# Kernel tuning notes

Measured on AMD Instinct MI355X. Metric: run time of the kernel, lower is better.

## Reference

```python
import jax, jax.numpy as jnp
import numpy as np

D = 768       # input_dim / model width
H = 3072      # expert hidden width (init arg 'output_dim')
E = 8         # num_experts
K = 2         # top_k
NOISE_STD = 0.1
B, S = 2, 1024


def setup_inputs() -> dict:
    key = jax.random.key(0)
    ks = jax.random.split(key, 16)
    sd = lambda fan_in: 1.0 / np.sqrt(fan_in)
    return {
        "x": jax.random.normal(ks[0], (B, S, D), dtype=jnp.float32),
        "noise": jax.random.normal(ks[1], (B, S, E), dtype=jnp.float32),
        # router
        "Wr": jax.random.normal(ks[2], (D, E), dtype=jnp.float32) * sd(D),
        "br": jnp.zeros((E,), dtype=jnp.float32),
        # stacked expert FFNs: d -> h -> d
        "W1": jax.random.normal(ks[3], (E, D, H), dtype=jnp.float32) * sd(D),
        "b1": jnp.zeros((E, H), dtype=jnp.float32),
        "W2": jax.random.normal(ks[4], (E, H, D), dtype=jnp.float32) * sd(H),
        "b2": jnp.zeros((E, D), dtype=jnp.float32),
        # shared expert
        "Ws1": jax.random.normal(ks[5], (D, H), dtype=jnp.float32) * sd(D),
        "bs1": jnp.zeros((H,), dtype=jnp.float32),
        "Ws2": jax.random.normal(ks[6], (H, D), dtype=jnp.float32) * sd(H),
        "bs2": jnp.zeros((D,), dtype=jnp.float32),
        # mixing scalars (alpha trainable, beta frozen in torch)
        "alpha": jnp.float32(0.3),
        "beta": jnp.float32(0.7),
    }


def reference(x, noise, Wr, br, W1, b1, W2, b2, Ws1, bs1, Ws2, bs2, alpha, beta):
    b, s, d = x.shape
    xt = x.reshape(-1, d)                       # [T, D]
    nt = noise.reshape(-1, E)                   # [T, E]
    T = xt.shape[0]

    # router: noisy logits -> top-k -> softmax over selected experts only
    logits = xt @ Wr + br + NOISE_STD * nt      # [T, E]
    top_vals, top_idx = jax.lax.top_k(logits, K)  # [T, K]
    top_w = jax.nn.softmax(top_vals, axis=-1)     # softmax over -inf-masked logits == softmax over top-k
    gates = jnp.zeros((T, E), dtype=x.dtype).at[jnp.arange(T)[:, None], top_idx].set(top_w)  # [T, E], 0 elsewhere

    # experts (dense over E; non-selected contributions are zeroed by gates)
    h = jax.nn.leaky_relu(jnp.einsum('td,edh->teh', xt, W1) + b1, negative_slope=0.01)  # [T, E, H]
    y = jnp.einsum('teh,ehd->ted', h, W2) + b2                                          # [T, E, D]
    moe_out = jnp.einsum('ted,te->td', y, gates)                                        # [T, D]

    # shared expert
    sh = jax.nn.leaky_relu(xt @ Ws1 + bs1, negative_slope=0.01)
    shared_out = sh @ Ws2 + bs2                                                         # [T, D]

    w = jax.nn.softmax(jnp.stack([alpha, beta]))
    out = shared_out * w[0] + moe_out * w[1]
    return out.reshape(b, s, d)
```

## Files before the change

kernel.cpp:

```cpp
#include <hip/hip_runtime.h>
#include <hip/hip_bf16.h>
#include <cstdio>
#include <cstdint>

#define TNUM 2048
#define DDIM 768
#define HDIM 3072
#define ENUM 8

#define WAITVM(N) asm volatile("s_waitcnt vmcnt(" #N ")" ::: "memory")
#define WAITLGKM() asm volatile("s_waitcnt lgkmcnt(0)" ::: "memory")
#define MEMFENCE() asm volatile("" ::: "memory")

typedef __attribute__((ext_vector_type(8))) __bf16 bf16x8;
typedef __attribute__((ext_vector_type(4))) float f32x4;

__device__ __forceinline__ unsigned short f2bf(float f) {
    __bf16 h = (__bf16)f;
    unsigned short u;
    __builtin_memcpy(&u, &h, 2);
    return u;
}

__device__ __forceinline__ void async_cp16(const unsigned short* g, unsigned short* l) {
    __builtin_amdgcn_global_load_lds((const __attribute__((address_space(1))) void*)g,
                                     (__attribute__((address_space(3))) void*)l,
                                     16, 0, 0);
}

__device__ __forceinline__ void transpose_tile(const float* __restrict__ in,
                                               unsigned short* __restrict__ out,
                                               int R, int C, int c0, int r0,
                                               unsigned int* tileT32) {
    int tid = threadIdx.x;
    int l15 = tid & 15;
    int g = tid >> 4;
    int par = (g >> 1) & 1;
    int hf = g & 1;
    int cb = hf * 64 + l15 * 4;
    const float* src = in + (size_t)(r0 + (g >> 1)) * C + c0 + cb;
    float4 v[16];
    #pragma unroll
    for (int p = 0; p < 16; p++)
        v[p] = *(const float4*)(src + (size_t)p * 8 * C);
    #pragma unroll
    for (int p = 0; p < 16; p++) {
        int unit = p * 16 + g;
        unsigned int m01 = (unsigned int)f2bf(v[p].x) | ((unsigned int)f2bf(v[p].y) << 16);
        unsigned int m23 = (unsigned int)f2bf(v[p].z) | ((unsigned int)f2bf(v[p].w) << 16);
        unsigned int o01 = __shfl_xor(m01, 32);
        unsigned int o23 = __shfl_xor(m23, 32);
        unsigned int wA = par ? ((o23 & 0xffffu) | (m23 << 16))
                              : ((m01 & 0xffffu) | (o01 << 16));
        unsigned int wB = par ? ((o23 >> 16) | (m23 & 0xffff0000u))
                              : ((m01 >> 16) | (o01 & 0xffff0000u));
        int ca = cb + par * 2;
        int rp = unit >> 2;
        int cq = ca >> 2;
        int woff = 4 * (((rp >> 2) + 3 * cq) & 15) + (((rp & 3) + cq) & 3);
        tileT32[ca * 68 + woff] = wA;
        tileT32[(ca + 1) * 68 + woff] = wB;
    }
    __syncthreads();
    uint4 Wv[8];
    #pragma unroll
    for (int p = 0; p < 8; p++) {
        int cc = p * 16 + g;
        int cqp = cc >> 2;
        Wv[p] = *(const uint4*)&tileT32[cc * 68 + 4 * ((l15 + 3 * cqp) & 15)];
    }
    #pragma unroll
    for (int p = 0; p < 8; p++) {
        int cc = p * 16 + g;
        int cqp = cc >> 2;
        unsigned int a0 = Wv[p].x, a1 = Wv[p].y, a2 = Wv[p].z, a3 = Wv[p].w;
        int rsel = cqp & 3;
        if (rsel & 1) { unsigned int t = a0; a0 = a1; a1 = a2; a2 = a3; a3 = t; }
        if (rsel & 2) { unsigned int t0 = a0, t1 = a1; a0 = a2; a1 = a3; a2 = t0; a3 = t1; }
        uint4 ov; ov.x = a0; ov.y = a1; ov.z = a2; ov.w = a3;
        *(uint4*)(out + (size_t)(c0 + cc) * R + r0 + l15 * 8) = ov;
    }
}

__global__ __launch_bounds__(256, 4)
void pre_kernel(const float* __restrict__ x, const float* __restrict__ noise,
                const float* __restrict__ Wr, const float* __restrict__ br,
                const float* __restrict__ W2, const float* __restrict__ Ws2,
                unsigned short* __restrict__ W2t, unsigned short* __restrict__ Ws2t,
                unsigned short* __restrict__ xb,
                int* __restrict__ counts, int* __restrict__ list,
                int* __restrict__ inv, float* __restrict__ tokp) {
    __shared__ __align__(16) unsigned int tileT32[128 * 68];
    int b = blockIdx.x;
    if (b < 1296) {
        int m = b / 144, t = b % 144;
        const float* in     = (m < 8) ? (W2 + (size_t)m * HDIM * DDIM) : Ws2;
        unsigned short* out = (m < 8) ? (W2t + (size_t)m * DDIM * HDIM) : Ws2t;
        transpose_tile(in, out, HDIM, DDIM, (t % 6) * 128, (t / 6) * 128, tileT32);
        return;
    }
    if (b < 2064) {
        int i = ((b - 1296) * 256 + threadIdx.x) * 8;
        float4 a = *(const float4*)(x + i);
        float4 bb = *(const float4*)(x + i + 4);
        ushort4 lo = make_ushort4(f2bf(a.x), f2bf(a.y), f2bf(a.z), f2bf(a.w));
        ushort4 hi = make_ushort4(f2bf(bb.x), f2bf(bb.y), f2bf(bb.z), f2bf(bb.w));
        *(ushort4*)(xb + i) = lo;
        *(ushort4*)(xb + i + 4) = hi;
        return;
    }
    int lane = threadIdx.x & 63;
    int t = (b - 2064) * 4 + (threadIdx.x >> 6);
    float acc[8];
    #pragma unroll
    for (int e = 0; e < 8; e++) acc[e] = 0.f;
    #pragma unroll
    for (int i = 0; i < 12; i++) {
        int d = i * 64 + lane;
        float xv = x[t * DDIM + d];
        float4 w0 = *(const float4*)(Wr + d * 8);
        float4 w1 = *(const float4*)(Wr + d * 8 + 4);
        acc[0] += xv * w0.x; acc[1] += xv * w0.y; acc[2] += xv * w0.z; acc[3] += xv * w0.w;
        acc[4] += xv * w1.x; acc[5] += xv * w1.y; acc[6] += xv * w1.z; acc[7] += xv * w1.w;
    }
    #pragma unroll
    for (int e = 0; e < 8; e++) {
        #pragma unroll
        for (int off2 = 32; off2 >= 1; off2 >>= 1)
            acc[e] += __shfl_xor(acc[e], off2, 64);
    }
    if (lane == 0) {
        float lg[8];
        #pragma unroll
        for (int e = 0; e < 8; e++) lg[e] = acc[e] + br[e] + 0.1f * noise[t * 8 + e];
        int e0 = 0;
        #pragma unroll
        for (int e = 1; e < 8; e++) if (lg[e] > lg[e0]) e0 = e;
        int e1 = -1;
        #pragma unroll
        for (int e = 0; e < 8; e++) if (e != e0 && (e1 < 0 || lg[e] > lg[e1])) e1 = e;
        float m = fmaxf(lg[e0], lg[e1]);
        float p0 = expf(lg[e0] - m), p1 = expf(lg[e1] - m);
        float inv_s = 1.f / (p0 + p1);
        int s0 = atomicAdd(&counts[e0], 1);
        list[e0 * TNUM + s0] = t;
        int s1 = atomicAdd(&counts[e1], 1);
        list[e1 * TNUM + s1] = t;
        inv[t * 2 + 0] = (e0 << 16) | s0;
        inv[t * 2 + 1] = (e1 << 16) | s1;
        tokp[t * 2 + 0] = p0 * inv_s;
        tokp[t * 2 + 1] = p1 * inv_s;
    }
}

__global__ __launch_bounds__(256, 3)
void ffn1_kernel(const unsigned short* __restrict__ xb,
                 const float* __restrict__ W1,
                 const float* __restrict__ Ws1,
                 const float* __restrict__ b1, const float* __restrict__ bs1,
                 const int* __restrict__ counts, const int* __restrict__ list,
                 unsigned short* __restrict__ hbuf) {
    __shared__ __align__(16) unsigned short As[2][512 * 8];
    __shared__ __align__(16) unsigned int Bs32[2048];

    int j = blockIdx.z * 8 + blockIdx.x;
    int y = blockIdx.y;
    int mt0 = y / 6, ntl = y % 6;

    int offv[8];
    { int s = 0;
      #pragma unroll
      for (int e = 0; e < 8; e++) { offv[e] = s; s += counts[e]; } }

    int cnt, hbase, n0, mbase, ntiles;
    const float* Bf;
    const float* bias;
    const int* lst = nullptr;
    if (j < 32) {
        int e = j >> 2, nq = j & 3;
        cnt = counts[e];
        ntiles = (cnt + 127) >> 7;
        mbase = 0;
        hbase = offv[e];
        n0 = nq * 768 + ntl * 128;
        Bf = W1 + (size_t)e * DDIM * HDIM;
        bias = b1 + e * HDIM;
        lst = list + e * TNUM;
    } else {
        int q = j - 32;
        int ms = q >> 2, nq = q & 3;
        mbase = ms * 512;
        ntiles = 4;
        cnt = 1 << 30;
        hbase = 2 * TNUM;
        n0 = nq * 768 + ntl * 128;
        Bf = Ws1;
        bias = bs1;
    }
    if (mt0 >= ntiles) return;

    int tid = threadIdx.x;
    int w = tid >> 6, lane = tid & 63;
    int l15 = lane & 15, quad = lane >> 4;
    int wm = (w & 1) * 64, wn = (w >> 1) * 64;
    int rcA = (w & 1) * 4;
    int rcB = (w >> 1) * 4;
    const int KT = DDIM / 32;

    int l31 = tid & 31;
    int rp0 = tid >> 5;
    int nlh = l31 >> 2;
    int nll4 = (l31 & 3) * 4;
    int c4 = l31 * 4;

    int ldsoff[2], rowl[2];
    #pragma unroll
    for (int r = 0; r < 2; r++) {
        int rc = r * 4 + w;
        rowl[r] = rc * 16 + l15;
        ldsoff[r] = rc * 512;
    }

    for (int mt = mt0; mt < ntiles; mt += 4) {
        int m0 = mbase + mt * 128;
        const unsigned short* gA[2];
        #pragma unroll
        for (int r = 0; r < 2; r++) {
            int row;
            if (lst) row = lst[min(m0 + rowl[r], cnt - 1)];
            else     row = m0 + rowl[r];
            gA[r] = xb + (size_t)row * DDIM + quad * 8;
        }

        f32x4 zero = {0.f, 0.f, 0.f, 0.f};
        f32x4 acc[4][4];
        #pragma unroll
        for (int i = 0; i < 4; i++)
            #pragma unroll
            for (int jj = 0; jj < 4; jj++) acc[i][jj] = zero;

        #pragma unroll
        for (int r = 0; r < 2; r++) async_cp16(gA[r], &As[0][ldsoff[r]]);
        float4 Ba[2], Bb[2];
        #pragma unroll
        for (int p = 0; p < 2; p++) {
            const float* bp = Bf + (size_t)(2 * (p * 8 + rp0)) * HDIM + n0 + c4;
            Ba[p] = *(const float4*)bp;
            Bb[p] = *(const float4*)(bp + HDIM);
        }

        #pragma unroll 1
        for (int kt = 0; kt < KT; kt++) {
            int cur = kt & 1;
            WAITVM(0);
            #pragma unroll
            for (int p = 0; p < 2; p++) {
                int kp = p * 8 + rp0;
                int gb = ((nlh * 64 + (kp >> 2) * 16 + nll4) << 2) + ((kp + nlh) & 3);
                float4 a = Ba[p], b = Bb[p];
                Bs32[gb + 0]  = (unsigned int)f2bf(a.x) | ((unsigned int)f2bf(b.x) << 16);
                Bs32[gb + 4]  = (unsigned int)f2bf(a.y) | ((unsigned int)f2bf(b.y) << 16);
                Bs32[gb + 8]  = (unsigned int)f2bf(a.z) | ((unsigned int)f2bf(b.z) << 16);
                Bs32[gb + 12] = (unsigned int)f2bf(a.w) | ((unsigned int)f2bf(b.w) << 16);
            }
            if (kt + 1 < KT) {
                int ko = (kt + 1) * 32;
                #pragma unroll
                for (int r = 0; r < 2; r++)
                    async_cp16(gA[r] + ko, &As[cur ^ 1][ldsoff[r]]);
                #pragma unroll
                for (int p = 0; p < 2; p++) {
                    const float* bp = Bf + (size_t)(ko + 2 * (p * 8 + rp0)) * HDIM + n0 + c4;
                    Ba[p] = *(const float4*)bp;
                    Bb[p] = *(const float4*)(bp + HDIM);
                }
            }
            WAITLGKM();
            __builtin_amdgcn_s_barrier();
            MEMFENCE();
            bf16x8 af[4], bv[4];
            #pragma unroll
            for (int i = 0; i < 4; i++)
                af[i] = *(const bf16x8*)&As[cur][((rcA + i) * 64 + quad * 16 + l15) * 8];
            #pragma unroll
            for (int jj = 0; jj < 4; jj++) {
                uint4 Wv = *(const uint4*)&Bs32[((rcB + jj) * 64 + quad * 16 + l15) << 2];
                unsigned int s0 = Wv.x, s1 = Wv.y, s2 = Wv.z, s3 = Wv.w;
                unsigned int t0, t1, t2, t3;
                if (jj == 0)      { t0 = s0; t1 = s1; t2 = s2; t3 = s3; }
                else if (jj == 1) { t0 = s1; t1 = s2; t2 = s3; t3 = s0; }
                else if (jj == 2) { t0 = s2; t1 = s3; t2 = s0; t3 = s1; }
                else              { t0 = s3; t1 = s0; t2 = s1; t3 = s2; }
                uint4 L; L.x = t0; L.y = t1; L.z = t2; L.w = t3;
                __builtin_memcpy(&bv[jj], &L, 16);
            }
            #pragma unroll
            for (int i = 0; i < 4; i++)
                #pragma unroll
                for (int jj = 0; jj < 4; jj++)
                    acc[i][jj] = __builtin_amdgcn_mfma_f32_16x16x32_bf16(af[i], bv[jj], acc[i][jj], 0, 0, 0);
            MEMFENCE();
            __builtin_amdgcn_s_barrier();
            MEMFENCE();
        }

        #pragma unroll
        for (int i = 0; i < 4; i++) {
            int rbase = m0 + wm + i * 16 + quad * 4;
            #pragma unroll
            for (int jj = 0; jj < 4; jj++) {
                int gc = n0 + wn + jj * 16 + l15;
                float bvl = bias[gc];
                #pragma unroll
                for (int r = 0; r < 4; r++) {
                    int gr = rbase + r;
                    if (gr < cnt) {
                        float v = acc[i][jj][r] + bvl;
                        v = v > 0.f ? v : 0.01f * v;
                        hbuf[(size_t)(hbase + gr) * HDIM + gc] = f2bf(v);
                    }
                }
            }
        }
    }
}

__global__ __launch_bounds__(256, 4)
void ffn2_kernel(const unsigned short* __restrict__ hbuf,
                 const unsigned short* __restrict__ W2t,
                 const unsigned short* __restrict__ Ws2t,
                 const int* __restrict__ counts,
                 float* __restrict__ ybuf) {
    __shared__ __align__(16) unsigned short As[2][512 * 8];
    __shared__ __align__(16) unsigned short Bs[2][512 * 8];

    int j = blockIdx.z * 8 + blockIdx.x;
    int y = blockIdx.y;
    int mt0 = y / 6, ntl = y % 6;
    int n0 = ntl * 128;

    int offv[8];
    { int s = 0;
      #pragma unroll
      for (int e = 0; e < 8; e++) { offv[e] = s; s += counts[e]; } }

    int cnt, hbase, mbase, kh, ntiles;
    const unsigned short* Bmat;
    if (j < 16) {
        int e = j >> 1; kh = j & 1;
        cnt = counts[e];
        ntiles = (cnt + 127) >> 7;
        mbase = 0;
        hbase = offv[e];
        Bmat = W2t + (size_t)e * DDIM * HDIM;
    } else {
        int q = j - 16;
        int ms = q >> 1; kh = q & 1;
        mbase = ms * 512;
        ntiles = 4;
        cnt = 1 << 30;
        hbase = 2 * TNUM;
        Bmat = Ws2t;
    }
    if (mt0 >= ntiles) return;
    int kbase = kh * (HDIM / 2);

    int tid = threadIdx.x;
    int w = tid >> 6, lane = tid & 63;
    int l15 = lane & 15, quad = lane >> 4;
    int wm = (w & 1) * 64, wn = (w >> 1) * 64;
    int rcA = (w & 1) * 4;
    int rcB = (w >> 1) * 4;
    const int KT = (HDIM / 2) / 32;

    const unsigned short* gB[2];
    int ldsoff[2], rowl[2];
    #pragma unroll
    for (int r = 0; r < 2; r++) {
        int rc = r * 4 + w;
        rowl[r] = rc * 16 + l15;
        ldsoff[r] = rc * 512;
        gB[r] = Bmat + (size_t)(n0 + rowl[r]) * HDIM + kbase + quad * 8;
    }
    float* yb = ybuf + (size_t)kh * 6144 * DDIM;

    for (int mt = mt0; mt < ntiles; mt += 4) {
        int m0 = mbase + mt * 128;
        const unsigned short* gA[2];
        #pragma unroll
        for (int r = 0; r < 2; r++) {
            int row = (j < 16) ? min(m0 + rowl[r], cnt - 1) : (m0 + rowl[r]);
            gA[r] = hbuf + (size_t)(hbase + row) * HDIM + kbase + quad * 8;
        }

        f32x4 zero = {0.f, 0.f, 0.f, 0.f};
        f32x4 acc[4][4];
        #pragma unroll
        for (int i = 0; i < 4; i++)
            #pragma unroll
            for (int jj = 0; jj < 4; jj++) acc[i][jj] = zero;

        #pragma unroll
        for (int t = 0; t < 2; t++)
            #pragma unroll
            for (int r = 0; r < 2; r++) {
                async_cp16(gA[r] + t * 32, &As[t][ldsoff[r]]);
                async_cp16(gB[r] + t * 32, &Bs[t][ldsoff[r]]);
            }

        #pragma unroll 1
        for (int kt = 0; kt < KT; kt++) {
            if (kt == KT - 1) { WAITVM(0); } else { WAITVM(4); }
            __builtin_amdgcn_s_barrier();
            MEMFENCE();
            int cur = kt & 1;
            bf16x8 af[4], bv[4];
            #pragma unroll
            for (int i = 0; i < 4; i++)
                af[i] = *(const bf16x8*)&As[cur][((rcA + i) * 64 + quad * 16 + l15) * 8];
            #pragma unroll
            for (int jj = 0; jj < 4; jj++)
                bv[jj] = *(const bf16x8*)&Bs[cur][((rcB + jj) * 64 + quad * 16 + l15) * 8];
            #pragma unroll
            for (int i = 0; i < 4; i++)
                #pragma unroll
                for (int jj = 0; jj < 4; jj++)
                    acc[i][jj] = __builtin_amdgcn_mfma_f32_16x16x32_bf16(af[i], bv[jj], acc[i][jj], 0, 0, 0);
            MEMFENCE();
            __builtin_amdgcn_s_barrier();
            MEMFENCE();
            if (kt + 2 < KT) {
                int ko = (kt + 2) * 32;
                #pragma unroll
                for (int r = 0; r < 2; r++) {
                    async_cp16(gA[r] + ko, &As[cur][ldsoff[r]]);
                    async_cp16(gB[r] + ko, &Bs[cur][ldsoff[r]]);
                }
            }
        }

        #pragma unroll
        for (int i = 0; i < 4; i++) {
            int rbase = m0 + wm + i * 16 + quad * 4;
            #pragma unroll
            for (int r = 0; r < 4; r++) {
                int gr = rbase + r;
                if (gr >= cnt) continue;
                float* orow = yb + (size_t)(hbase + gr) * DDIM + n0 + wn;
                #pragma unroll
                for (int jj = 0; jj < 4; jj++)
                    orow[jj * 16 + l15] = acc[i][jj][r];
            }
        }
    }
}

__global__ void mix_kernel(const float* __restrict__ ybuf, const int* __restrict__ inv,
                           const float* __restrict__ tokp, const int* __restrict__ counts,
                           const float* __restrict__ b2, const float* __restrict__ bs2,
                           const float* __restrict__ alpha, const float* __restrict__ beta,
                           float* __restrict__ out) {
    int t = blockIdx.x;
    int c = threadIdx.x * 4;
    int offv[8];
    { int s = 0;
      #pragma unroll
      for (int e = 0; e < 8; e++) { offv[e] = s; s += counts[e]; } }
    float a = alpha[0], bsc = beta[0];
    float m = fmaxf(a, bsc);
    float ea = expf(a - m), eb = expf(bsc - m);
    float is = 1.f / (ea + eb);
    float ws = ea * is, wmx = eb * is;

    int i0 = inv[t * 2 + 0], i1 = inv[t * 2 + 1];
    int e0 = i0 >> 16, sl0 = i0 & 0xFFFF;
    int e1 = i1 >> 16, sl1 = i1 & 0xFFFF;
    float p0 = tokp[t * 2 + 0], p1 = tokp[t * 2 + 1];
    size_t rA = (size_t)(offv[e0] + sl0) * DDIM + c;
    size_t rB = (size_t)(offv[e1] + sl1) * DDIM + c;
    size_t rS = (size_t)(2 * TNUM + t) * DDIM + c;
    const float* y0 = ybuf;
    const float* y1 = ybuf + (size_t)6144 * DDIM;
    float4 vA0 = *(const float4*)(y0 + rA);
    float4 vA1 = *(const float4*)(y1 + rA);
    float4 vB0 = *(const float4*)(y0 + rB);
    float4 vB1 = *(const float4*)(y1 + rB);
    float4 vS0 = *(const float4*)(y0 + rS);
    float4 vS1 = *(const float4*)(y1 + rS);
    float4 bA = *(const float4*)(b2 + e0 * DDIM + c);
    float4 bB = *(const float4*)(b2 + e1 * DDIM + c);
    float4 bS = *(const float4*)(bs2 + c);
    float4 o;
    o.x = ws * (vS0.x + vS1.x + bS.x) + wmx * (p0 * (vA0.x + vA1.x + bA.x) + p1 * (vB0.x + vB1.x + bB.x));
    o.y = ws * (vS0.y + vS1.y + bS.y) + wmx * (p0 * (vA0.y + vA1.y + bA.y) + p1 * (vB0.y + vB1.y + bB.y));
    o.z = ws * (vS0.z + vS1.z + bS.z) + wmx * (p0 * (vA0.z + vA1.z + bA.z) + p1 * (vB0.z + vB1.z + bB.z));
    o.w = ws * (vS0.w + vS1.w + bS.w) + wmx * (p0 * (vA0.w + vA1.w + bA.w) + p1 * (vB0.w + vB1.w + bB.w));
    *(float4*)(out + (size_t)t * DDIM + c) = o;
}

extern "C" void kernel_launch(void* const* d_in, const int* in_sizes, int n_in,
                              void* d_out, int out_size, void* d_ws, size_t ws_size,
                              hipStream_t stream) {
    const float* x     = (const float*)d_in[0];
    const float* noise = (const float*)d_in[1];
    const float* Wr    = (const float*)d_in[2];
    const float* br    = (const float*)d_in[3];
    const float* W1    = (const float*)d_in[4];
    const float* b1    = (const float*)d_in[5];
    const float* W2    = (const float*)d_in[6];
    const float* b2    = (const float*)d_in[7];
    const float* Ws1   = (const float*)d_in[8];
    const float* bs1   = (const float*)d_in[9];
    const float* Ws2   = (const float*)d_in[10];
    const float* bs2   = (const float*)d_in[11];
    const float* alpha = (const float*)d_in[12];
    const float* beta  = (const float*)d_in[13];

    char* ws = (char*)d_ws;
    size_t off = 0;
    auto alloc = [&](size_t bytes) -> char* {
        char* p = ws + off;
        off = (off + bytes + 255) & ~(size_t)255;
        return p;
    };
    int*   counts = (int*)  alloc(ENUM * 4);
    int*   list   = (int*)  alloc((size_t)ENUM * TNUM * 4);
    int*   inv    = (int*)  alloc((size_t)TNUM * 2 * 4);
    float* tokp   = (float*)alloc((size_t)TNUM * 2 * 4);
    unsigned short* xb   = (unsigned short*)alloc((size_t)TNUM * DDIM * 2);
    float* ybuf          = (float*)alloc((size_t)2 * 6144 * DDIM * 4);
    unsigned short* W2t  = (unsigned short*)alloc((size_t)ENUM * DDIM * HDIM * 2);
    unsigned short* Ws2t = (unsigned short*)alloc((size_t)DDIM * HDIM * 2);
    unsigned short* hbuf = (unsigned short*)alloc((size_t)(3 * TNUM) * HDIM * 2);
    if (off > ws_size) {
        fprintf(stderr, "kernel_launch: workspace too small (need %zu, have %zu)\n", off, ws_size);
        return;
    }

    hipMemsetAsync(counts, 0, ENUM * 4, stream);

    pre_kernel<<<dim3(2576), dim3(256), 0, stream>>>(x, noise, Wr, br, W2, Ws2,
                                                     W2t, Ws2t, xb, counts, list, inv, tokp);
    ffn1_kernel<<<dim3(8, 24, 6), dim3(256), 0, stream>>>(xb, W1, Ws1, b1, bs1, counts, list, hbuf);
    ffn2_kernel<<<dim3(8, 24, 3), dim3(256), 0, stream>>>(hbuf, W2t, Ws2t, counts, ybuf);
    mix_kernel<<<dim3(TNUM), dim3(192), 0, stream>>>(ybuf, inv, tokp, counts, b2, bs2,
                                                     alpha, beta, (float*)d_out);
}
```

Baseline: 415.8 us.

## Double-buffer B tile in LDS and prefetch fp32 weights two stages ahead

The ffn1 kernel now keeps two LDS buffers for the converted bf16 B tile. Global fp32 weight loads are issued two k-steps ahead and converted into the next buffer while the current one feeds the MFMAs. Fine-grained vmcnt waits replace the full drain at the top of each iteration, so weight-load latency overlaps compute. The cost is extra LDS (8 KB), which may lower occupancy under the launch bounds, plus waitcnt counts that depend on exact instruction ordering.

```diff
diff --git a/kernel.cpp b/kernel.cpp
--- a/kernel.cpp
+++ b/kernel.cpp
@@ -161,7 +161,7 @@
                  const int* __restrict__ counts, const int* __restrict__ list,
                  unsigned short* __restrict__ hbuf) {
     __shared__ __align__(16) unsigned short As[2][512 * 8];
-    __shared__ __align__(16) unsigned int Bs32[2048];
+    __shared__ __align__(16) unsigned int Bs32[2][2048];
 
     int j = blockIdx.z * 8 + blockIdx.x;
     int y = blockIdx.y;
@@ -239,8 +239,6 @@
             #pragma unroll
             for (int jj = 0; jj < 4; jj++) acc[i][jj] = zero;
 
-        #pragma unroll
-        for (int r = 0; r < 2; r++) async_cp16(gA[r], &As[0][ldsoff[r]]);
         float4 Ba[2], Bb[2];
         #pragma unroll
         for (int p = 0; p < 2; p++) {
@@ -248,33 +246,63 @@
             Ba[p] = *(const float4*)bp;
             Bb[p] = *(const float4*)(bp + HDIM);
         }
+        WAITVM(0);
+        #pragma unroll
+        for (int p = 0; p < 2; p++) {
+            int kp = p * 8 + rp0;
+            int gb = ((nlh * 64 + (kp >> 2) * 16 + nll4) << 2) + ((kp + nlh) & 3);
+            float4 a = Ba[p], b = Bb[p];
+            Bs32[0][gb + 0]  = (unsigned int)f2bf(a.x) | ((unsigned int)f2bf(b.x) << 16);
+            Bs32[0][gb + 4]  = (unsigned int)f2bf(a.y) | ((unsigned int)f2bf(b.y) << 16);
+            Bs32[0][gb + 8]  = (unsigned int)f2bf(a.z) | ((unsigned int)f2bf(b.z) << 16);
+            Bs32[0][gb + 12] = (unsigned int)f2bf(a.w) | ((unsigned int)f2bf(b.w) << 16);
+        }
+        MEMFENCE();
+        #pragma unroll
+        for (int p = 0; p < 2; p++) {
+            const float* bp = Bf + (size_t)(32 + 2 * (p * 8 + rp0)) * HDIM + n0 + c4;
+            Ba[p] = *(const float4*)bp;
+            Bb[p] = *(const float4*)(bp + HDIM);
+        }
+        MEMFENCE();
+        #pragma unroll
+        for (int r = 0; r < 2; r++) async_cp16(gA[r], &As[0][ldsoff[r]]);
 
         #pragma unroll 1
         for (int kt = 0; kt < KT; kt++) {
             int cur = kt & 1;
-            WAITVM(0);
-            #pragma unroll
-            for (int p = 0; p < 2; p++) {
-                int kp = p * 8 + rp0;
-                int gb = ((nlh * 64 + (kp >> 2) * 16 + nll4) << 2) + ((kp + nlh) & 3);
-                float4 a = Ba[p], b = Bb[p];
-                Bs32[gb + 0]  = (unsigned int)f2bf(a.x) | ((unsigned int)f2bf(b.x) << 16);
-                Bs32[gb + 4]  = (unsigned int)f2bf(a.y) | ((unsigned int)f2bf(b.y) << 16);
-                Bs32[gb + 8]  = (unsigned int)f2bf(a.z) | ((unsigned int)f2bf(b.z) << 16);
-                Bs32[gb + 12] = (unsigned int)f2bf(a.w) | ((unsigned int)f2bf(b.w) << 16);
-            }
             if (kt + 1 < KT) {
-                int ko = (kt + 1) * 32;
-                #pragma unroll
-                for (int r = 0; r < 2; r++)
-                    async_cp16(gA[r] + ko, &As[cur ^ 1][ldsoff[r]]);
+                WAITVM(2);
+                #pragma unroll
+                for (int p = 0; p < 2; p++) {
+                    int kp = p * 8 + rp0;
+                    int gb = ((nlh * 64 + (kp >> 2) * 16 + nll4) << 2) + ((kp + nlh) & 3);
+                    float4 a = Ba[p], b = Bb[p];
+                    Bs32[cur ^ 1][gb + 0]  = (unsigned int)f2bf(a.x) | ((unsigned int)f2bf(b.x) << 16);
+                    Bs32[cur ^ 1][gb + 4]  = (unsigned int)f2bf(a.y) | ((unsigned int)f2bf(b.y) << 16);
+                    Bs32[cur ^ 1][gb + 8]  = (unsigned int)f2bf(a.z) | ((unsigned int)f2bf(b.z) << 16);
+                    Bs32[cur ^ 1][gb + 12] = (unsigned int)f2bf(a.w) | ((unsigned int)f2bf(b.w) << 16);
+                }
+            }
+            if (kt + 2 < KT) {
+                int ko = (kt + 2) * 32;
                 #pragma unroll
                 for (int p = 0; p < 2; p++) {
                     const float* bp = Bf + (size_t)(ko + 2 * (p * 8 + rp0)) * HDIM + n0 + c4;
                     Ba[p] = *(const float4*)bp;
                     Bb[p] = *(const float4*)(bp + HDIM);
                 }
-            }
+                MEMFENCE();
+            }
+            if (kt + 1 < KT) {
+                int ka = (kt + 1) * 32;
+                #pragma unroll
+                for (int r = 0; r < 2; r++)
+                    async_cp16(gA[r] + ka, &As[cur ^ 1][ldsoff[r]]);
+            }
+            if (kt + 2 < KT)      { WAITVM(6); }
+            else if (kt + 1 < KT) { WAITVM(2); }
+            else                  { WAITVM(0); }
             WAITLGKM();
             __builtin_amdgcn_s_barrier();
             MEMFENCE();
@@ -284,7 +312,7 @@
                 af[i] = *(const bf16x8*)&As[cur][((rcA + i) * 64 + quad * 16 + l15) * 8];
             #pragma unroll
             for (int jj = 0; jj < 4; jj++) {
-                uint4 Wv = *(const uint4*)&Bs32[((rcB + jj) * 64 + quad * 16 + l15) << 2];
+                uint4 Wv = *(const uint4*)&Bs32[cur][((rcB + jj) * 64 + quad * 16 + l15) << 2];
                 unsigned int s0 = Wv.x, s1 = Wv.y, s2 = Wv.z, s3 = Wv.w;
                 unsigned int t0, t1, t2, t3;
                 if (jj == 0)      { t0 = s0; t1 = s1; t2 = s2; t3 = s3; }
```

Measured after the change: 411.5 us. No clear change (-1.0%).
